# Kernel optimization log

Hardware: AMD Instinct MI355X
Metric: run time of the kernel (lower is better)

Reference implementation:

```python
import jax, jax.numpy as jnp
import numpy as np

DIM = 100

def setup_inputs() -> dict:
    key = jax.random.key(0)
    k1, k2, k3, k4, k5, k6 = jax.random.split(key, 6)
    n_items, B, L = 50000, 1024, 200
    item_embedding = jax.random.normal(k1, (n_items, DIM), dtype=jnp.float32)
    items = jax.random.randint(k2, (B, L), 0, n_items, dtype=jnp.int64)
    A = jax.random.uniform(k3, (B, B), dtype=jnp.float32)
    D = jax.random.uniform(k4, (B, B), dtype=jnp.float32)
    session_len = jax.random.uniform(k5, (B, 1), minval=1.0, maxval=float(L), dtype=jnp.float32)
    target_embedding = jax.random.normal(k6, (B, DIM), dtype=jnp.float32)
    return {"item_embedding": item_embedding, "items": items, "A": A, "D": D,
            "session_len": session_len, "target_embedding": target_embedding}

def reference(item_embedding, items, A, D, session_len, target_embedding):
    # Prepend a zero row (padding index 0 in the original torch code)
    emb = jnp.concatenate([jnp.zeros((1, item_embedding.shape[1]), item_embedding.dtype),
                           item_embedding], axis=0)          # [n+1, dim]
    seq_h = emb[items]                                        # [B, L, dim] gather
    rel = jnp.sum(seq_h, axis=1) / session_len                # [B, dim] mean-pool
    DA = jnp.matmul(D, A)                                     # [B, B]
    rel = jnp.matmul(DA, rel)                                 # [B, dim] propagation
    c = jax.nn.selu(rel)                                      # [B, dim]
    l_c = c / jnp.linalg.norm(c, axis=-1, keepdims=True)      # L2 normalize rows
    return l_c
```

## Files before the change

### kernel.cpp

```cpp
#include <hip/hip_runtime.h>
#include <math.h>

#define B_   1024
#define L_   200
#define DIM_ 100
#define NP   128
#define K_   1024
#define NCH  16
#define KCH  (K_ / NCH)

__global__ __launch_bounds__(256) void gather_pool_k(
    const float* __restrict__ emb, const int* __restrict__ items,
    const float* __restrict__ slen, float4* __restrict__ relP4) {
  const int b = blockIdx.x;
  const int t = threadIdx.x;
  const int s = t >> 5;
  const int c = t & 31;
  const int* __restrict__ row = items + b * L_;
  float4 acc = make_float4(0.f, 0.f, 0.f, 0.f);
  if (c < 25) {
    #pragma unroll
    for (int j = 0; j < L_ / 8; ++j) {
      const int idx = row[s + 8 * j];
      if (idx > 0) {
        const float4 v = *(const float4*)&emb[(size_t)(idx - 1) * DIM_ + c * 4];
        acc.x += v.x; acc.y += v.y; acc.z += v.z; acc.w += v.w;
      }
    }
  }
  __shared__ float4 sm[8][32];
  sm[s][c] = acc;
  __syncthreads();
  if (s < 4) {
    float4 o = sm[s + 4][c];
    sm[s][c].x += o.x; sm[s][c].y += o.y; sm[s][c].z += o.z; sm[s][c].w += o.w;
  }
  __syncthreads();
  if (s < 2) {
    float4 o = sm[s + 2][c];
    sm[s][c].x += o.x; sm[s][c].y += o.y; sm[s][c].z += o.z; sm[s][c].w += o.w;
  }
  __syncthreads();
  if (s == 0) {
    float4 a0 = sm[0][c], a1 = sm[1][c];
    const float inv = 1.f / slen[b];
    float4 r;
    r.x = (a0.x + a1.x) * inv; r.y = (a0.y + a1.y) * inv;
    r.z = (a0.z + a1.z) * inv; r.w = (a0.w + a1.w) * inv;
    relP4[b * 32 + c] = (c < 25) ? r : make_float4(0.f, 0.f, 0.f, 0.f);
  }
}

#define BM 32
__global__ __launch_bounds__(256) void gemm_splitk_k(
    const float* __restrict__ A,
    const float* __restrict__ Bm,
    float* __restrict__ Cpart) {
  __shared__ float As[BM][KCH];
  __shared__ float Bs[KCH][NP];
  const int t   = threadIdx.x;
  const int m0  = blockIdx.x * BM;
  const int k0  = blockIdx.y * KCH;
  const int tc  = t & 31;
  const int tr  = t >> 5;

  #pragma unroll
  for (int q = 0; q < 2; ++q) {
    const int f = t + q * 256;
    const int r = f >> 4, kk = (f & 15) * 4;
    *(float4*)&As[r][kk] = *(const float4*)&A[(size_t)(m0 + r) * K_ + (k0 + kk)];
  }
  #pragma unroll
  for (int q = 0; q < 8; ++q) {
    const int f = t + q * 256;
    const int r = f >> 5, c = (f & 31) * 4;
    *(float4*)&Bs[r][c] = *(const float4*)&Bm[(size_t)(k0 + r) * NP + c];
  }
  __syncthreads();

  float acc[4][4] = {};
  #pragma unroll
  for (int kk4 = 0; kk4 < KCH; kk4 += 4) {
    float a[4][4], bb[4][4];
    #pragma unroll
    for (int i = 0; i < 4; ++i)
      *(float4*)a[i] = *(const float4*)&As[tr * 4 + i][kk4];
    #pragma unroll
    for (int j = 0; j < 4; ++j)
      *(float4*)bb[j] = *(const float4*)&Bs[kk4 + j][tc * 4];
    #pragma unroll
    for (int j = 0; j < 4; ++j)
      #pragma unroll
      for (int i = 0; i < 4; ++i)
        #pragma unroll
        for (int c = 0; c < 4; ++c)
          acc[i][c] += a[i][j] * bb[j][c];
  }

  float* Cc = Cpart + (size_t)blockIdx.y * B_ * NP;
  #pragma unroll
  for (int i = 0; i < 4; ++i)
    *(float4*)&Cc[(size_t)(m0 + tr * 4 + i) * NP + tc * 4] = *(float4*)acc[i];
}

__global__ __launch_bounds__(256) void reduce_k(
    const float* __restrict__ part, float* __restrict__ outm) {
  const int i4 = blockIdx.x * 256 + threadIdx.x;
  const float4* p = (const float4*)part;
  float4 v = p[i4];
  #pragma unroll
  for (int c = 1; c < NCH; ++c) {
    float4 w = p[(size_t)c * (B_ * NP / 4) + i4];
    v.x += w.x; v.y += w.y; v.z += w.z; v.w += w.w;
  }
  ((float4*)outm)[i4] = v;
}

__global__ __launch_bounds__(128) void epilogue_k(
    const float* __restrict__ prePart, float* __restrict__ out) {
  const int b = blockIdx.x, c = threadIdx.x;
  float x = 0.f;
  #pragma unroll
  for (int p = 0; p < NCH; ++p)
    x += prePart[(size_t)p * B_ * NP + b * NP + c];
  const float scale = 1.0507009873554804934f;
  const float alpha = 1.6732632423543772848f;
  float s = (x > 0.f) ? (scale * x) : (scale * alpha * expm1f(x));
  if (c >= DIM_) s = 0.f;
  float ss = s * s;
  #pragma unroll
  for (int off = 32; off > 0; off >>= 1) ss += __shfl_down(ss, off, 64);
  __shared__ float wsum[2];
  if ((c & 63) == 0) wsum[c >> 6] = ss;
  __syncthreads();
  const float inv = 1.f / sqrtf(wsum[0] + wsum[1]);
  if (c < DIM_) out[b * DIM_ + c] = s * inv;
}

extern "C" void kernel_launch(void* const* d_in, const int* in_sizes, int n_in,
                              void* d_out, int out_size, void* d_ws, size_t ws_size,
                              hipStream_t stream) {
  const float* emb   = (const float*)d_in[0];
  const int*   items = (const int*)d_in[1];
  const float* A     = (const float*)d_in[2];
  const float* D     = (const float*)d_in[3];
  const float* slen  = (const float*)d_in[4];
  float* out = (float*)d_out;

  char* ws = (char*)d_ws;
  const size_t matB = (size_t)B_ * NP * sizeof(float);
  float* relP    = (float*)(ws);
  float* tPart   = (float*)(ws + 1 * matB);
  float* tM      = (float*)(ws + 17 * matB);
  float* prePart = (float*)(ws + 18 * matB);

  gather_pool_k<<<B_, 256, 0, stream>>>(emb, items, slen, (float4*)relP);
  gemm_splitk_k<<<dim3(B_ / BM, NCH), 256, 0, stream>>>(A, relP, tPart);
  reduce_k<<<B_ * NP / 4 / 256, 256, 0, stream>>>(tPart, tM);
  gemm_splitk_k<<<dim3(B_ / BM, NCH), 256, 0, stream>>>(D, tM, prePart);
  epilogue_k<<<B_, 128, 0, stream>>>(prePart, out);
}
```

Measured before the change: 111.3 us.

## Replace split-K partial buffers with atomic accumulation and fuse epilogue via last-block counter

The split-K GEMMs now accumulate directly into one output matrix with float atomicAdd, which removes the separate reduce kernel and the 16 partial-buffer writes and reads. The SELU and L2-normalize epilogue is fused into the second GEMM: a per-tile arrival counter lets the last block of each row tile apply the activation. Zeroing of the accumulators and the counter is folded into the gather kernel. This drops two kernel launches and a lot of memory traffic. In exchange it adds many scalar atomics, and the summation order becomes nondeterministic.

```diff
diff --git a/kernel.cpp b/kernel.cpp
--- a/kernel.cpp
+++ b/kernel.cpp
@@ -1,21 +1,31 @@
 #include <hip/hip_runtime.h>
 #include <math.h>
 
-#define B_   1024
-#define L_   200
-#define DIM_ 100
-#define NP   128
-#define K_   1024
-#define NCH  16
-#define KCH  (K_ / NCH)
+#define B_    1024
+#define L_    200
+#define DIM_  100
+#define NP    128
+#define K_    1024
+#define NCH   16
+#define KCH   (K_ / NCH)
+#define BM    32
+#define NTILE (B_ / BM)
 
 __global__ __launch_bounds__(256) void gather_pool_k(
     const float* __restrict__ emb, const int* __restrict__ items,
-    const float* __restrict__ slen, float4* __restrict__ relP4) {
+    const float* __restrict__ slen, float4* __restrict__ relP4,
+    float4* __restrict__ tM4, float4* __restrict__ preM4,
+    int* __restrict__ cnt) {
   const int b = blockIdx.x;
   const int t = threadIdx.x;
   const int s = t >> 5;
   const int c = t & 31;
+  if (t < 32) {
+    const float4 z = make_float4(0.f, 0.f, 0.f, 0.f);
+    tM4[b * 32 + t] = z;
+    preM4[b * 32 + t] = z;
+    if (b == 0) cnt[t] = 0;
+  }
   const int* __restrict__ row = items + b * L_;
   float4 acc = make_float4(0.f, 0.f, 0.f, 0.f);
   if (c < 25) {
@@ -51,18 +61,20 @@
   }
 }
 
-#define BM 32
+template <int FINAL>
 __global__ __launch_bounds__(256) void gemm_splitk_k(
     const float* __restrict__ A,
     const float* __restrict__ Bm,
-    float* __restrict__ Cpart) {
+    float* __restrict__ C,
+    int* __restrict__ cnt,
+    float* __restrict__ out) {
   __shared__ float As[BM][KCH];
   __shared__ float Bs[KCH][NP];
-  const int t   = threadIdx.x;
-  const int m0  = blockIdx.x * BM;
-  const int k0  = blockIdx.y * KCH;
-  const int tc  = t & 31;
-  const int tr  = t >> 5;
+  const int t  = threadIdx.x;
+  const int m0 = blockIdx.x * BM;
+  const int k0 = blockIdx.y * KCH;
+  const int tc = t & 31;
+  const int tr = t >> 5;
 
   #pragma unroll
   for (int q = 0; q < 2; ++q) {
@@ -73,8 +85,8 @@
   #pragma unroll
   for (int q = 0; q < 8; ++q) {
     const int f = t + q * 256;
-    const int r = f >> 5, c = (f & 31) * 4;
-    *(float4*)&Bs[r][c] = *(const float4*)&Bm[(size_t)(k0 + r) * NP + c];
+    const int r = f >> 5, cc = (f & 31) * 4;
+    *(float4*)&Bs[r][cc] = *(const float4*)&Bm[(size_t)(k0 + r) * NP + cc];
   }
   __syncthreads();
 
@@ -93,48 +105,47 @@
       #pragma unroll
       for (int i = 0; i < 4; ++i)
         #pragma unroll
-        for (int c = 0; c < 4; ++c)
-          acc[i][c] += a[i][j] * bb[j][c];
+        for (int q = 0; q < 4; ++q)
+          acc[i][q] += a[i][j] * bb[j][q];
   }
 
-  float* Cc = Cpart + (size_t)blockIdx.y * B_ * NP;
   #pragma unroll
   for (int i = 0; i < 4; ++i)
-    *(float4*)&Cc[(size_t)(m0 + tr * 4 + i) * NP + tc * 4] = *(float4*)acc[i];
-}
+    #pragma unroll
+    for (int q = 0; q < 4; ++q)
+      atomicAdd(&C[(size_t)(m0 + tr * 4 + i) * NP + tc * 4 + q], acc[i][q]);
 
-__global__ __launch_bounds__(256) void reduce_k(
-    const float* __restrict__ part, float* __restrict__ outm) {
-  const int i4 = blockIdx.x * 256 + threadIdx.x;
-  const float4* p = (const float4*)part;
-  float4 v = p[i4];
-  #pragma unroll
-  for (int c = 1; c < NCH; ++c) {
-    float4 w = p[(size_t)c * (B_ * NP / 4) + i4];
-    v.x += w.x; v.y += w.y; v.z += w.z; v.w += w.w;
-  }
-  ((float4*)outm)[i4] = v;
-}
+  if (!FINAL) return;
 
-__global__ __launch_bounds__(128) void epilogue_k(
-    const float* __restrict__ prePart, float* __restrict__ out) {
-  const int b = blockIdx.x, c = threadIdx.x;
-  float x = 0.f;
-  #pragma unroll
-  for (int p = 0; p < NCH; ++p)
-    x += prePart[(size_t)p * B_ * NP + b * NP + c];
+  __threadfence();
+  __shared__ int lastFlag;
+  if (t == 0) lastFlag = (atomicAdd(&cnt[blockIdx.x], 1) == NCH - 1);
+  __syncthreads();
+  if (!lastFlag) return;
+  __threadfence();
+
   const float scale = 1.0507009873554804934f;
   const float alpha = 1.6732632423543772848f;
-  float s = (x > 0.f) ? (scale * x) : (scale * alpha * expm1f(x));
-  if (c >= DIM_) s = 0.f;
-  float ss = s * s;
   #pragma unroll
-  for (int off = 32; off > 0; off >>= 1) ss += __shfl_down(ss, off, 64);
-  __shared__ float wsum[2];
-  if ((c & 63) == 0) wsum[c >> 6] = ss;
-  __syncthreads();
-  const float inv = 1.f / sqrtf(wsum[0] + wsum[1]);
-  if (c < DIM_) out[b * DIM_ + c] = s * inv;
+  for (int rr = 0; rr < 4; ++rr) {
+    const int row = m0 + tr * 4 + rr;
+    const float4 x = *(const float4*)&C[(size_t)row * NP + tc * 4];
+    float4 sv;
+    sv.x = (x.x > 0.f) ? scale * x.x : scale * alpha * expm1f(x.x);
+    sv.y = (x.y > 0.f) ? scale * x.y : scale * alpha * expm1f(x.y);
+    sv.z = (x.z > 0.f) ? scale * x.z : scale * alpha * expm1f(x.z);
+    sv.w = (x.w > 0.f) ? scale * x.w : scale * alpha * expm1f(x.w);
+    float ss = (tc < 25) ? (sv.x*sv.x + sv.y*sv.y + sv.z*sv.z + sv.w*sv.w) : 0.f;
+    #pragma unroll
+    for (int off = 16; off > 0; off >>= 1)
+      ss += __shfl_xor(ss, off, 64);
+    const float inv = 1.f / sqrtf(ss);
+    if (tc < 25) {
+      float4 o;
+      o.x = sv.x * inv; o.y = sv.y * inv; o.z = sv.z * inv; o.w = sv.w * inv;
+      *(float4*)&out[(size_t)row * DIM_ + tc * 4] = o;
+    }
+  }
 }
 
 extern "C" void kernel_launch(void* const* d_in, const int* in_sizes, int n_in,
@@ -149,14 +160,13 @@
 
   char* ws = (char*)d_ws;
   const size_t matB = (size_t)B_ * NP * sizeof(float);
-  float* relP    = (float*)(ws);
-  float* tPart   = (float*)(ws + 1 * matB);
-  float* tM      = (float*)(ws + 17 * matB);
-  float* prePart = (float*)(ws + 18 * matB);
+  float* relP = (float*)(ws);
+  float* tM   = (float*)(ws + 1 * matB);
+  float* preM = (float*)(ws + 2 * matB);
+  int*   cnt  = (int*)(ws + 3 * matB);
 
-  gather_pool_k<<<B_, 256, 0, stream>>>(emb, items, slen, (float4*)relP);
-  gemm_splitk_k<<<dim3(B_ / BM, NCH), 256, 0, stream>>>(A, relP, tPart);
-  reduce_k<<<B_ * NP / 4 / 256, 256, 0, stream>>>(tPart, tM);
-  gemm_splitk_k<<<dim3(B_ / BM, NCH), 256, 0, stream>>>(D, tM, prePart);
-  epilogue_k<<<B_, 128, 0, stream>>>(prePart, out);
+  gather_pool_k<<<B_, 256, 0, stream>>>(emb, items, slen, (float4*)relP,
+                                        (float4*)tM, (float4*)preM, cnt);
+  gemm_splitk_k<0><<<dim3(NTILE, NCH), 256, 0, stream>>>(A, relP, tM, cnt, out);
+  gemm_splitk_k<1><<<dim3(NTILE, NCH), 256, 0, stream>>>(D, tM, preM, cnt, out);
 }
```

Measured after the change: 175.3 us. +57.5%, slower.
